# Kernel tuning notes

Hardware: AMD Instinct MI355X
Metric: run time of the kernel (lower is better)

## Reference

```python
import jax, jax.numpy as jnp
import numpy as np

# ---- static config (mirrors module init / config constants) ----
STATE_DIM = 512
D_H = 2048
INPUT_DIM = 1024
N_QUBITS = 6
N_VQC_LAYERS = 3
MSD = 128                 # mamba_state_dim (last dim of padded state)
PAD_SLICES = 16           # padded slice count in h_padded
MIN_T = 1e-6              # control_limits.min_value
REL_STEP = 0.1            # control_limits.hardware_relative_step
ABS_STEP = 1e-4           # control_limits.hardware_absolute_step
MAX_T = 0.05              # control_limits.max_value
DIM = 2 ** N_QUBITS

# qubit 0 = most significant bit (matches reshape-based gate application)
_BITS = ((np.arange(DIM)[:, None] >> np.arange(N_QUBITS)[None, ::-1]) & 1).astype(np.float32)
_sign = np.ones(DIM, np.float32)
for k in range(N_QUBITS):  # ring CZ entanglement
    k2 = (k + 1) % N_QUBITS
    _sign *= 1.0 - 2.0 * _BITS[:, k] * _BITS[:, k2]
CZ_SIGN = jnp.asarray(_sign)
Z_OBS = jnp.asarray((1.0 - 2.0 * _BITS).mean(axis=1))  # mean <Z_k> observable weights


def _apply_ry(state, ang, k):
    # state: [B, 2^n] real statevector; ang: [B] rotation angle on qubit k
    B = state.shape[0]
    s = state.reshape(B, 2 ** k, 2, 2 ** (N_QUBITS - k - 1))
    c = jnp.cos(ang / 2)[:, None, None]
    si = jnp.sin(ang / 2)[:, None, None]
    a0, a1 = s[:, :, 0, :], s[:, :, 1, :]
    out = jnp.stack([c * a0 - si * a1, si * a0 + c * a1], axis=2)
    return out.reshape(B, DIM)


def _vqc(feats, enc_W, enc_b, thetas):
    # EvolutionTimeVQCLayer: angle-encode features, layered RY + ring CZ, mean-Z expectation
    B = feats.shape[0]
    angles = feats @ enc_W + enc_b  # [B, n_qubits]
    state = jnp.zeros((B, DIM), feats.dtype).at[:, 0].set(1.0)
    for k in range(N_QUBITS):
        state = _apply_ry(state, angles[:, k], k)
    for l in range(N_VQC_LAYERS):
        for k in range(N_QUBITS):
            state = _apply_ry(state, jnp.broadcast_to(thetas[l, k], (B,)), k)
        state = state * CZ_SIGN[None, :]
    return (state * state) @ Z_OBS  # [B]


def _hamiltonian(q, p, x, W1, b1, W2, b2, W3, b3):
    z = jnp.concatenate([q, p, x], axis=-1)          # [B, 2*S + D]
    h1 = jnp.tanh(z @ W1 + b1)
    h2 = jnp.tanh(h1 @ W2 + b2)
    return (h2 @ W3)[:, 0] + b3                       # [B] scalar energy per sample


def setup_inputs() -> dict:
    key = jax.random.key(0)
    ks = jax.random.split(key, 12)
    def glorot(k, shape):
        std = np.sqrt(2.0 / (shape[0] + shape[-1]))
        return jax.random.normal(k, shape, jnp.float32) * std
    B = 2048
    h_in = 2 * STATE_DIM + INPUT_DIM
    gen_in = INPUT_DIM + 2 * STATE_DIM
    return {
        'x': jax.random.normal(ks[0], (B, INPUT_DIM), jnp.float32),
        'h_padded': jax.random.normal(ks[1], (B, PAD_SLICES, MSD), jnp.float32),
        'aux_padded': jnp.zeros((B, PAD_SLICES, MSD), jnp.float32),
        'W1': glorot(ks[2], (h_in, D_H)), 'b1': jnp.zeros((D_H,), jnp.float32),
        'W2': glorot(ks[3], (D_H, D_H)), 'b2': jnp.zeros((D_H,), jnp.float32),
        'W3': glorot(ks[4], (D_H, 1)), 'b3': jnp.zeros((), jnp.float32),
        'W_out': glorot(ks[5], (2 * STATE_DIM, INPUT_DIM)),
        'b_out': jnp.zeros((INPUT_DIM,), jnp.float32),
        'enc_W': glorot(ks[6], (gen_in, N_QUBITS)) * 0.1,
        'enc_b': jnp.zeros((N_QUBITS,), jnp.float32),
        'thetas': jax.random.normal(ks[7], (N_VQC_LAYERS, N_QUBITS), jnp.float32) * 0.1,
        'gain': jnp.asarray(0.1, jnp.float32),
        'shift': jnp.asarray(7.0, jnp.float32),
        'cap_param': jnp.asarray(0.02, jnp.float32),
        'time_bias': jnp.asarray(0.0005, jnp.float32),
        'last_stable': jnp.asarray(0.0005, jnp.float32),
    }


def reference(x, h_padded, aux_padded, W1, b1, W2, b2, W3, b3, W_out, b_out,
              enc_W, enc_b, thetas, gain, shift, cap_param, time_bias, last_stable):
    B = x.shape[0]
    total = 2 * STATE_DIM
    num_slices = total // MSD
    # unpack phase-space state from padded mamba-shaped state
    unpacked = h_padded[:, :num_slices, :].reshape(B, total)
    q_t, p_t = jnp.split(unpacked, 2, axis=-1)

    # ---- evolution-time generation via VQC ----
    ctrl = jnp.concatenate([x, q_t, p_t], axis=-1)
    samples = _vqc(ctrl, enc_W, enc_b, thetas)                       # [B]
    soft_gain = jax.nn.softplus(gain)
    soft_shift = jax.nn.softplus(shift)
    adjusted = jax.nn.softplus(soft_gain * samples - soft_shift)
    raw = jnp.mean(adjusted) + time_bias
    cap = jnp.maximum(jax.nn.softplus(cap_param), 1e-6)
    evo = cap * jax.nn.sigmoid(raw / cap)
    evo = jnp.where(jnp.isfinite(evo), evo, cap * jax.nn.sigmoid(time_bias / cap))
    prev = jnp.maximum(last_stable, MIN_T)
    cand = jnp.maximum(evo, MIN_T)
    max_step = jnp.maximum(prev * REL_STEP, ABS_STEP)
    cand = jnp.minimum(cand, prev + max_step)
    cand = jnp.minimum(cand, MAX_T)
    dt = jnp.where(jnp.isfinite(cand), cand, prev)                   # scalar

    # ---- fused HNN symplectic (leapfrog) step ----
    def H_sum(q, p):
        return _hamiltonian(q, p, x, W1, b1, W2, b2, W3, b3).sum()
    grad_qp = jax.grad(H_sum, argnums=(0, 1))
    dHdq0, _ = grad_qp(q_t, p_t)
    p_half = p_t - 0.5 * dt * dHdq0
    _, dHdp_h = grad_qp(q_t, p_half)
    q_next = q_t + dt * dHdp_h
    dHdq_n, _ = grad_qp(q_next, p_half)
    p_next = p_half - 0.5 * dt * dHdq_n

    out = jnp.concatenate([q_next, p_next], axis=-1) @ W_out + b_out  # [B, INPUT_DIM]

    # repack state into padded mamba layout
    new_slices = jnp.concatenate([q_next, p_next], axis=-1).reshape(B, num_slices, MSD)
    pad = jnp.zeros((B, PAD_SLICES - num_slices, MSD), out.dtype)
    h_next = jnp.concatenate([new_slices, pad], axis=1)
    return out, h_next
```

## Files before the change

kernel.cpp:

```cpp
#include <hip/hip_runtime.h>
#include <math.h>

#define NB 2048
#define ZD 2048
#define SD 512
#define NELEM_Z (NB * ZD)
#define MB_ (1024 * 1024)

typedef float f32x4 __attribute__((ext_vector_type(4)));
typedef __bf16 bf16x8 __attribute__((ext_vector_type(8)));
typedef __bf16 bf16x4 __attribute__((ext_vector_type(4)));
typedef long long i64;

__device__ __forceinline__ float softplus_f(float x) {
  if (x > 20.f) return x;
  if (x < -20.f) return expf(x);
  return log1pf(expf(x));
}

__device__ __forceinline__ void gload_lds16(const __bf16* g, __bf16* l) {
  __builtin_amdgcn_global_load_lds(
      (__attribute__((address_space(1))) void*)(g),
      (__attribute__((address_space(3))) void*)(l), 16, 0, 0);
}

__device__ __forceinline__ int pack_fp8x4(float a, float b, float c, float d) {
  int p = __builtin_amdgcn_cvt_pk_fp8_f32(a, b, 0, false);
  p = __builtin_amdgcn_cvt_pk_fp8_f32(c, d, p, true);
  return p;
}
__device__ __forceinline__ float fp8_to_f32(unsigned char b) {
  return __builtin_amdgcn_cvt_f32_fp8((int)b, 0);
}

__global__ __launch_bounds__(256) void build_z_kernel(
    const float* __restrict__ x,
    const float* __restrict__ h_padded,
    const float* __restrict__ enc_W,
    const float* __restrict__ enc_b,
    float* __restrict__ z,
    __bf16* __restrict__ zb,
    unsigned char* __restrict__ zf8,
    float* __restrict__ angles,
    float* __restrict__ acc) {
  int b = blockIdx.x;
  int tid = threadIdx.x;
  if (b == 0 && tid == 0) acc[0] = 0.f;
  int lane = tid & 63, w = tid >> 6;
  __shared__ float red[4][6];

  float pa[6] = {0.f, 0.f, 0.f, 0.f, 0.f, 0.f};
#pragma unroll
  for (int cc = 0; cc < 2; cc++) {
    int c = cc * 256 + tid;
    int i = c * 4;
    f32x4 v = (i < 1024) ? ((const f32x4*)(h_padded + (size_t)b * 2048))[c]
                         : ((const f32x4*)(x + (size_t)b * 1024))[c - 256];
    size_t zi = (size_t)b * 512 + c;
    ((f32x4*)z)[zi] = v;
    bf16x4 o;
    o[0] = (__bf16)v[0]; o[1] = (__bf16)v[1];
    o[2] = (__bf16)v[2]; o[3] = (__bf16)v[3];
    ((bf16x4*)zb)[zi] = o;
    ((int*)zf8)[zi] = pack_fp8x4(v[0], v[1], v[2], v[3]);
    int cj = (i < 1024) ? (1024 + i) : (i - 1024);
#pragma unroll
    for (int e = 0; e < 4; e++) {
      const float* wp = enc_W + (size_t)(cj + e) * 6;
#pragma unroll
      for (int k = 0; k < 6; k++) pa[k] += v[e] * wp[k];
    }
  }
#pragma unroll
  for (int k = 0; k < 6; k++)
    for (int off = 32; off > 0; off >>= 1) pa[k] += __shfl_down(pa[k], off, 64);
  if (lane == 0) {
#pragma unroll
    for (int k = 0; k < 6; k++) red[w][k] = pa[k];
  }
  __syncthreads();
  if (tid < 6)
    angles[b * 6 + tid] =
        red[0][tid] + red[1][tid] + red[2][tid] + red[3][tid] + enc_b[tid];
}

__global__ void prep_w(const float* __restrict__ in,
                       __bf16* __restrict__ outT, int R, int C) {
  __shared__ float tile[32][33];
  int bx = blockIdx.x * 32, by = blockIdx.y * 32;
  int tx = threadIdx.x, ty = threadIdx.y;
  for (int r = ty; r < 32; r += 8)
    tile[r][tx] = in[(size_t)(by + r) * C + bx + tx];
  __syncthreads();
  for (int r = ty; r < 32; r += 8)
    outT[(size_t)(bx + r) * R + by + tx] = (__bf16)tile[tx][r];
}

__global__ void prep_w8(const float* __restrict__ in,
                        unsigned char* __restrict__ outN,
                        unsigned char* __restrict__ outT, int R, int C) {
  __shared__ float tile[32][33];
  int bx = blockIdx.x * 32, by = blockIdx.y * 32;
  int tx = threadIdx.x, ty = threadIdx.y;
  for (int r = ty; r < 32; r += 8) {
    float v = in[(size_t)(by + r) * C + bx + tx] * 16.f;
    tile[r][tx] = v;
    int p = __builtin_amdgcn_cvt_pk_fp8_f32(v, v, 0, false);
    outN[(size_t)(by + r) * C + bx + tx] = (unsigned char)(p & 0xff);
  }
  __syncthreads();
  for (int r = ty; r < 32; r += 8) {
    float v = tile[tx][r];
    int p = __builtin_amdgcn_cvt_pk_fp8_f32(v, v, 0, false);
    outT[(size_t)(bx + r) * R + by + tx] = (unsigned char)(p & 0xff);
  }
}

__global__ __launch_bounds__(64) void sim_kernel(
    const float* __restrict__ angles,
    const float* __restrict__ thetas,
    const float* __restrict__ gain,
    const float* __restrict__ shift,
    float* __restrict__ acc) {
  int row = blockIdx.x * 64 + threadIdx.x;
  const float* a = angles + row * 6;

  float s[64];
#pragma unroll
  for (int i = 0; i < 64; i++) s[i] = 0.f;
  s[0] = 1.f;

#pragma unroll
  for (int k = 0; k < 6; k++) {
    float half = 0.5f * a[k];
    float c = cosf(half), si = sinf(half);
    int m = 1 << (5 - k);
#pragma unroll
    for (int i = 0; i < 64; i++) {
      if ((i & m) == 0) {
        float a0 = s[i], a1 = s[i | m];
        s[i] = c * a0 - si * a1;
        s[i | m] = si * a0 + c * a1;
      }
    }
  }
#pragma unroll
  for (int l = 0; l < 3; l++) {
#pragma unroll
    for (int k = 0; k < 6; k++) {
      float half = 0.5f * thetas[l * 6 + k];
      float c = cosf(half), si = sinf(half);
      int m = 1 << (5 - k);
#pragma unroll
      for (int i = 0; i < 64; i++) {
        if ((i & m) == 0) {
          float a0 = s[i], a1 = s[i | m];
          s[i] = c * a0 - si * a1;
          s[i | m] = si * a0 + c * a1;
        }
      }
    }
#pragma unroll
    for (int i = 0; i < 64; i++) {
      int rot = ((i << 1) | (i >> 5)) & 63;
      if (__popc(i & rot) & 1) s[i] = -s[i];
    }
  }

  float val = 0.f;
#pragma unroll
  for (int i = 0; i < 64; i++) {
    float zo = (6.f - 2.f * (float)__popc(i)) * (1.f / 6.f);
    val += s[i] * s[i] * zo;
  }
  float sg = softplus_f(gain[0]);
  float ss = softplus_f(shift[0]);
  float adj = softplus_f(sg * val - ss);
  for (int off = 32; off > 0; off >>= 1) adj += __shfl_down(adj, off, 64);
  if (threadIdx.x == 0) atomicAdd(acc, adj);
}

__global__ void dt_kernel(const float* __restrict__ acc,
                          const float* __restrict__ cap_param,
                          const float* __restrict__ time_bias,
                          const float* __restrict__ last_stable,
                          float* __restrict__ dt_out) {
  float raw = acc[0] * (1.f / (float)NB) + time_bias[0];
  float cap = fmaxf(softplus_f(cap_param[0]), 1e-6f);
  float evo = cap / (1.f + expf(-raw / cap));
  if (!isfinite(evo)) evo = cap / (1.f + expf(-time_bias[0] / cap));
  float prev = fmaxf(last_stable[0], 1e-6f);
  float cand = fmaxf(evo, 1e-6f);
  float max_step = fmaxf(prev * 0.1f, 1e-4f);
  cand = fminf(cand, prev + max_step);
  cand = fminf(cand, 0.05f);
  dt_out[0] = isfinite(cand) ? cand : prev;
}

template <int EPI>
__global__ __launch_bounds__(256, 2) void mfma_gemm8(
    const unsigned char* __restrict__ A, int lda,
    const unsigned char* __restrict__ Bt, int ldb,
    void* __restrict__ Cv, int ldc,
    const float* __restrict__ bias,
    const float* __restrict__ w3,
    const unsigned char* __restrict__ aux, int ldaux,
    int Kslice) {
  __shared__ __align__(16) unsigned char sA[2][128 * 144];
  __shared__ __align__(16) unsigned char sB[2][64 * 144];

  const int tid = threadIdx.x;
  const int lane = tid & 63;
  const int w = tid >> 6;
  const int wm = w & 1, wn = w >> 1;
  const int row0 = blockIdx.y * 128;
  const int col0 = blockIdx.x * 64;
  const int koff = blockIdx.z * Kslice;

  const unsigned char* gA[4]; int wA0[4], wA1[4];
  const unsigned char* gB[2]; int wB0[2], wB1[2];
#pragma unroll
  for (int i = 0; i < 4; i++) {
    int c = i * 256 + tid;
    int m = c >> 3, cp = c & 7;
    gA[i] = A + (size_t)(row0 + m) * lda + koff + cp * 16;
    int h = cp >> 1;
    int Hofs = (h >> 1) * 16 + (h & 1) * 8;
    wA0[i] = m * 144 + ((2 * cp) & 3) * 32 + Hofs;
    wA1[i] = m * 144 + ((2 * cp + 1) & 3) * 32 + Hofs;
  }
#pragma unroll
  for (int i = 0; i < 2; i++) {
    int c = i * 256 + tid;
    int m = c >> 3, cp = c & 7;
    gB[i] = Bt + (size_t)(col0 + m) * ldb + koff + cp * 16;
    int h = cp >> 1;
    int Hofs = (h >> 1) * 16 + (h & 1) * 8;
    wB0[i] = m * 144 + ((2 * cp) & 3) * 32 + Hofs;
    wB1[i] = m * 144 + ((2 * cp + 1) & 3) * 32 + Hofs;
  }

  const int q = lane >> 4, r = lane & 15;
  int aoff[4][2], boff[2][2];
#pragma unroll
  for (int i = 0; i < 4; i++) {
    int ma = wm * 64 + i * 16 + r;
#pragma unroll
    for (int H = 0; H < 2; H++) aoff[i][H] = ma * 144 + q * 32 + H * 16;
  }
#pragma unroll
  for (int j = 0; j < 2; j++) {
    int mb = wn * 32 + j * 16 + r;
#pragma unroll
    for (int H = 0; H < 2; H++) boff[j][H] = mb * 144 + q * 32 + H * 16;
  }

  f32x4 acc[4][2] = {};
  f32x4 rA[4], rB[2];

#pragma unroll
  for (int i = 0; i < 4; i++) rA[i] = *(const f32x4*)gA[i];
#pragma unroll
  for (int i = 0; i < 2; i++) rB[i] = *(const f32x4*)gB[i];
#pragma unroll
  for (int i = 0; i < 4; i++) {
    *(i64*)(&sA[0][0] + wA0[i]) = ((const i64*)&rA[i])[0];
    *(i64*)(&sA[0][0] + wA1[i]) = ((const i64*)&rA[i])[1];
  }
#pragma unroll
  for (int i = 0; i < 2; i++) {
    *(i64*)(&sB[0][0] + wB0[i]) = ((const i64*)&rB[i])[0];
    *(i64*)(&sB[0][0] + wB1[i]) = ((const i64*)&rB[i])[1];
  }
  __syncthreads();

  int cur = 0;
  for (int k0 = 0; k0 < Kslice; k0 += 128) {
    const bool more = (k0 + 128 < Kslice);
    if (more) {
#pragma unroll
      for (int i = 0; i < 4; i++) rA[i] = *(const f32x4*)(gA[i] + k0 + 128);
#pragma unroll
      for (int i = 0; i < 2; i++) rB[i] = *(const f32x4*)(gB[i] + k0 + 128);
    }

    const unsigned char* bA = &sA[cur][0];
    const unsigned char* bB = &sB[cur][0];
#pragma unroll
    for (int H = 0; H < 2; H++) {
      i64 a0[4], a1[4], b0[2], b1[2];
#pragma unroll
      for (int i = 0; i < 4; i++) {
        f32x4 v = *(const f32x4*)(bA + aoff[i][H]);
        a0[i] = ((const i64*)&v)[0];
        a1[i] = ((const i64*)&v)[1];
      }
#pragma unroll
      for (int j = 0; j < 2; j++) {
        f32x4 v = *(const f32x4*)(bB + boff[j][H]);
        b0[j] = ((const i64*)&v)[0];
        b1[j] = ((const i64*)&v)[1];
      }
#pragma unroll
      for (int i = 0; i < 4; i++)
#pragma unroll
        for (int j = 0; j < 2; j++)
          acc[i][j] = __builtin_amdgcn_mfma_f32_16x16x32_fp8_fp8(
              a0[i], b0[j], acc[i][j], 0, 0, 0);
#pragma unroll
      for (int i = 0; i < 4; i++)
#pragma unroll
        for (int j = 0; j < 2; j++)
          acc[i][j] = __builtin_amdgcn_mfma_f32_16x16x32_fp8_fp8(
              a1[i], b1[j], acc[i][j], 0, 0, 0);
    }

    if (more) {
      unsigned char* nA = &sA[cur ^ 1][0];
      unsigned char* nB = &sB[cur ^ 1][0];
#pragma unroll
      for (int i = 0; i < 4; i++) {
        *(i64*)(nA + wA0[i]) = ((const i64*)&rA[i])[0];
        *(i64*)(nA + wA1[i]) = ((const i64*)&rA[i])[1];
      }
#pragma unroll
      for (int i = 0; i < 2; i++) {
        *(i64*)(nB + wB0[i]) = ((const i64*)&rB[i])[0];
        *(i64*)(nB + wB1[i]) = ((const i64*)&rB[i])[1];
      }
    }
    __syncthreads();
    cur ^= 1;
  }

  float* Cf = (float*)Cv;
  unsigned char* C8 = (unsigned char*)Cv;
  float* Pz = Cf + (size_t)blockIdx.z * (size_t)gridDim.y * 128 * ldc;

#pragma unroll
  for (int i = 0; i < 4; i++) {
    int rowb = row0 + wm * 64 + i * 16 + q * 4;
#pragma unroll
    for (int j = 0; j < 2; j++) {
      int col = col0 + wn * 32 + j * 16 + r;
      if (EPI == 0) {
#pragma unroll
        for (int g = 0; g < 4; g++)
          Pz[(size_t)(rowb + g) * ldc + col] = acc[i][j][g];
      } else {
        float o[4];
#pragma unroll
        for (int g = 0; g < 4; g++) {
          float v = acc[i][j][g] * 0.0625f;
          if (EPI == 1) {
            o[g] = tanhf(v + bias[col]);
          } else if (EPI == 2) {
            float t = tanhf(v + bias[col]);
            o[g] = 32.f * (1.f - t * t) * w3[col];
          } else {
            float h = fp8_to_f32(aux[(size_t)(rowb + g) * ldaux + col]);
            o[g] = v * (1.f - h * h);
          }
        }
        int p = pack_fp8x4(o[0], o[1], o[2], o[3]);
#pragma unroll
        for (int g = 0; g < 4; g++)
          C8[(size_t)(rowb + g) * ldc + col] =
              (unsigned char)((p >> (8 * g)) & 0xff);
      }
    }
  }
}

__global__ __launch_bounds__(256, 2) void mfma_gemm_bf16(
    const __bf16* __restrict__ A, int lda,
    const __bf16* __restrict__ Bt, int ldb,
    float* __restrict__ P, int ldc,
    int Kslice) {
  __shared__ __bf16 sA[2][128 * 64];
  __shared__ __bf16 sB[2][64 * 64];

  const int tid = threadIdx.x;
  const int lane = tid & 63;
  const int w = tid >> 6;
  const int wm = w & 1, wn = w >> 1;
  const int row0 = blockIdx.y * 128;
  const int col0 = blockIdx.x * 64;
  const int koff = blockIdx.z * Kslice;

  const __bf16* gA[4]; int lofA[4];
  const __bf16* gB[2]; int lofB[2];
#pragma unroll
  for (int i = 0; i < 4; i++) {
    int c = i * 256 + tid;
    int m = c >> 3, cc = c & 7;
    int o = cc ^ (m & 7);
    gA[i] = A + (size_t)(row0 + m) * lda + koff + o * 8;
    lofA[i] = c * 8;
  }
#pragma unroll
  for (int i = 0; i < 2; i++) {
    int c = i * 256 + tid;
    int m = c >> 3, cc = c & 7;
    int o = cc ^ (m & 7);
    gB[i] = Bt + (size_t)(col0 + m) * ldb + koff + o * 8;
    lofB[i] = c * 8;
  }

  const int q = lane >> 4, r = lane & 15;
  int aoff[4][2], boff[2][2];
#pragma unroll
  for (int i = 0; i < 4; i++) {
    int ma = wm * 64 + i * 16 + r;
#pragma unroll
    for (int h = 0; h < 2; h++)
      aoff[i][h] = (ma * 8 + ((h * 4 + q) ^ (ma & 7))) * 8;
  }
#pragma unroll
  for (int j = 0; j < 2; j++) {
    int mb = wn * 32 + j * 16 + r;
#pragma unroll
    for (int h = 0; h < 2; h++)
      boff[j][h] = (mb * 8 + ((h * 4 + q) ^ (mb & 7))) * 8;
  }

  f32x4 acc[4][2] = {};

#pragma unroll
  for (int i = 0; i < 4; i++) gload_lds16(gA[i], &sA[0][0] + lofA[i]);
#pragma unroll
  for (int i = 0; i < 2; i++) gload_lds16(gB[i], &sB[0][0] + lofB[i]);

  int cur = 0;
  for (int k0 = 0; k0 < Kslice; k0 += 64) {
    __syncthreads();
    if (k0 + 64 < Kslice) {
      int nxt = cur ^ 1;
#pragma unroll
      for (int i = 0; i < 4; i++)
        gload_lds16(gA[i] + k0 + 64, &sA[nxt][0] + lofA[i]);
#pragma unroll
      for (int i = 0; i < 2; i++)
        gload_lds16(gB[i] + k0 + 64, &sB[nxt][0] + lofB[i]);
    }
#pragma unroll
    for (int h = 0; h < 2; h++) {
      bf16x8 af[4], bfr[2];
#pragma unroll
      for (int i = 0; i < 4; i++)
        af[i] = *(const bf16x8*)(&sA[cur][0] + aoff[i][h]);
#pragma unroll
      for (int j = 0; j < 2; j++)
        bfr[j] = *(const bf16x8*)(&sB[cur][0] + boff[j][h]);
#pragma unroll
      for (int i = 0; i < 4; i++)
#pragma unroll
        for (int j = 0; j < 2; j++)
          acc[i][j] = __builtin_amdgcn_mfma_f32_16x16x32_bf16(af[i], bfr[j],
                                                              acc[i][j], 0, 0, 0);
    }
    cur ^= 1;
  }

  float* Pz = P + (size_t)blockIdx.z * (size_t)gridDim.y * 128 * ldc;
#pragma unroll
  for (int i = 0; i < 4; i++) {
    int rowb = row0 + wm * 64 + i * 16 + q * 4;
#pragma unroll
    for (int j = 0; j < 2; j++) {
      int col = col0 + wn * 32 + j * 16 + r;
#pragma unroll
      for (int g = 0; g < 4; g++)
        Pz[(size_t)(rowb + g) * ldc + col] = acc[i][j][g];
    }
  }
}

__global__ void update_kernel(float* __restrict__ z, __bf16* __restrict__ zb,
                              unsigned char* __restrict__ zf8,
                              const float* __restrict__ gp,
                              const float* __restrict__ dt,
                              float coef, int off) {
  int t = blockIdx.x * blockDim.x + threadIdx.x;
  int b = t >> 7;
  int j4 = t & 127;
  const f32x4* g4 = (const f32x4*)gp;
  constexpr int STRIDE = NB * SD / 4;
  f32x4 g = g4[t] + g4[t + STRIDE] + g4[t + 2 * STRIDE] + g4[t + 3 * STRIDE];
  int zi4 = (b * ZD + off) / 4 + j4;
  f32x4 v = ((f32x4*)z)[zi4];
  float s = coef * dt[0] * (1.f / 512.f);
  v[0] += s * g[0]; v[1] += s * g[1]; v[2] += s * g[2]; v[3] += s * g[3];
  ((f32x4*)z)[zi4] = v;
  bf16x4 o;
  o[0] = (__bf16)v[0]; o[1] = (__bf16)v[1];
  o[2] = (__bf16)v[2]; o[3] = (__bf16)v[3];
  ((bf16x4*)zb)[zi4] = o;
  ((int*)zf8)[zi4] = pack_fp8x4(v[0], v[1], v[2], v[3]);
}

__global__ void wout_reduce(const float* __restrict__ gp,
                            const float* __restrict__ b_out,
                            float* __restrict__ out) {
  int t = blockIdx.x * blockDim.x + threadIdx.x;
  constexpr int S = NB * 1024 / 4;
  const f32x4* g4 = (const f32x4*)gp;
  f32x4 v = g4[t] + g4[t + S];
  f32x4 bb = ((const f32x4*)b_out)[t & 255];
  v[0] += bb[0]; v[1] += bb[1]; v[2] += bb[2]; v[3] += bb[3];
  ((f32x4*)out)[t] = v;
}

__global__ void hnext_kernel(const float* __restrict__ z,
                             float* __restrict__ out) {
  int t = blockIdx.x * blockDim.x + threadIdx.x;
  int i4 = t & 511;
  f32x4 zero = {0.f, 0.f, 0.f, 0.f};
  ((f32x4*)out)[t] = (i4 < 256) ? ((const f32x4*)z)[t] : zero;
}

extern "C" void kernel_launch(void* const* d_in, const int* in_sizes, int n_in,
                              void* d_out, int out_size, void* d_ws,
                              size_t ws_size, hipStream_t stream) {
  const float* x        = (const float*)d_in[0];
  const float* h_padded = (const float*)d_in[1];
  const float* W1    = (const float*)d_in[3];
  const float* b1    = (const float*)d_in[4];
  const float* W2    = (const float*)d_in[5];
  const float* b2    = (const float*)d_in[6];
  const float* W3    = (const float*)d_in[7];
  const float* W_out = (const float*)d_in[9];
  const float* b_out = (const float*)d_in[10];
  const float* enc_W = (const float*)d_in[11];
  const float* enc_b = (const float*)d_in[12];
  const float* thetas = (const float*)d_in[13];
  const float* gain   = (const float*)d_in[14];
  const float* shift  = (const float*)d_in[15];
  const float* cap_p  = (const float*)d_in[16];
  const float* t_bias = (const float*)d_in[17];
  const float* l_stab = (const float*)d_in[18];

  float* out_mat  = (float*)d_out;
  float* out_hnxt = (float*)d_out + NB * 1024;

  char* base = (char*)d_ws;
  float* z      = (float*)(base);
  float* part   = (float*)(base + 16 * MB_);
  __bf16* zb    = (__bf16*)(base + 32 * MB_);
  __bf16* Wot   = (__bf16*)(base + 40 * MB_);
  float* angl   = (float*)(base + 42 * MB_);
  float* accp   = (float*)(base + 42 * MB_ + 65536);
  float* dtp    = accp + 1;
  unsigned char* zf8  = (unsigned char*)(base + 43 * MB_);
  unsigned char* h1_8 = zf8 + (size_t)NELEM_Z;
  unsigned char* g2_8 = h1_8 + (size_t)NELEM_Z;
  unsigned char* g1_8 = g2_8 + (size_t)NELEM_Z;
  unsigned char* W1n8 = g1_8 + (size_t)NELEM_Z;
  unsigned char* W1t8 = W1n8 + (size_t)NELEM_Z;
  unsigned char* W2n8 = W1t8 + (size_t)NELEM_Z;
  unsigned char* W2t8 = W2n8 + (size_t)NELEM_Z;

  dim3 thr256(256);
  dim3 thrT(32, 8);

  prep_w8<<<dim3(64, 64), thrT, 0, stream>>>(W1, W1n8, W1t8, ZD, ZD);
  prep_w8<<<dim3(64, 64), thrT, 0, stream>>>(W2, W2n8, W2t8, ZD, ZD);
  prep_w<<<dim3(32, 32), thrT, 0, stream>>>(W_out, Wot, 1024, 1024);

  build_z_kernel<<<dim3(NB), thr256, 0, stream>>>(x, h_padded, enc_W, enc_b, z,
                                                  zb, zf8, angl, accp);
  sim_kernel<<<dim3(NB / 64), dim3(64), 0, stream>>>(angl, thetas, gain, shift,
                                                     accp);
  dt_kernel<<<dim3(1), dim3(1), 0, stream>>>(accp, cap_p, t_bias, l_stab, dtp);

  const int   j0r[3]  = {0, 512, 0};
  const int   offs[3] = {512, 0, 512};
  const float coef[3] = {-0.5f, 1.0f, -0.5f};

  dim3 gridSq(32, 16, 1);
  dim3 gridGr(8, 16, 4);

  for (int i = 0; i < 3; i++) {
    mfma_gemm8<1><<<gridSq, thr256, 0, stream>>>(
        zf8, ZD, W1t8, ZD, h1_8, ZD, b1, nullptr, nullptr, 0, ZD);
    mfma_gemm8<2><<<gridSq, thr256, 0, stream>>>(
        h1_8, ZD, W2t8, ZD, g2_8, ZD, b2, W3, nullptr, 0, ZD);
    mfma_gemm8<3><<<gridSq, thr256, 0, stream>>>(
        g2_8, ZD, W2n8, ZD, g1_8, ZD, nullptr, nullptr, h1_8, ZD, ZD);
    mfma_gemm8<0><<<gridGr, thr256, 0, stream>>>(
        g1_8, ZD, W1n8 + (size_t)j0r[i] * ZD, ZD, part, SD, nullptr, nullptr,
        nullptr, 0, 512);
    update_kernel<<<dim3(NB * SD / 4 / 256), thr256, 0, stream>>>(
        z, zb, zf8, part, dtp, coef[i], offs[i]);
  }

  mfma_gemm_bf16<<<dim3(16, 16, 2), thr256, 0, stream>>>(zb, ZD, Wot, 1024,
                                                         part, 1024, 512);
  wout_reduce<<<dim3(NB * 1024 / 4 / 256), thr256, 0, stream>>>(part, b_out,
                                                                out_mat);

  hnext_kernel<<<dim3(NELEM_Z / 4 / 256), thr256, 0, stream>>>(z, out_hnxt);
}
```

Measured before the change: 447.1 us.

## Use MX-scaled 16x16x128 FP8 MFMA with XOR-swizzled unpadded LDS tiles

Replaces the pairs of 16x16x32 FP8 MFMAs with the gfx950 scaled 16x16x128 f8f6f4 MFMA, using neutral scale exponents, so each k-tile needs one matrix instruction per output fragment. The LDS layout moves from 144-byte padded rows with split 8-byte stores to 128-byte rows with an XOR swizzle, which allows single 16-byte stores and reads. This is meant to cut MFMA issue count and LDS instruction overhead. It depends on the operand lane/K mapping of the new instruction matching the swizzled layout, or the results will be wrong.

```diff
diff --git a/kernel.cpp b/kernel.cpp
--- a/kernel.cpp
+++ b/kernel.cpp
@@ -10,6 +10,8 @@
 typedef float f32x4 __attribute__((ext_vector_type(4)));
 typedef __bf16 bf16x8 __attribute__((ext_vector_type(8)));
 typedef __bf16 bf16x4 __attribute__((ext_vector_type(4)));
+typedef int i32x4 __attribute__((ext_vector_type(4)));
+typedef int i32x8 __attribute__((ext_vector_type(8)));
 typedef long long i64;
 
 __device__ __forceinline__ float softplus_f(float x) {
@@ -206,8 +208,8 @@
     const float* __restrict__ w3,
     const unsigned char* __restrict__ aux, int ldaux,
     int Kslice) {
-  __shared__ __align__(16) unsigned char sA[2][128 * 144];
-  __shared__ __align__(16) unsigned char sB[2][64 * 144];
+  __shared__ __align__(16) unsigned char sA[2][128 * 128];
+  __shared__ __align__(16) unsigned char sB[2][64 * 128];
 
   const int tid = threadIdx.x;
   const int lane = tid & 63;
@@ -217,27 +219,21 @@
   const int col0 = blockIdx.x * 64;
   const int koff = blockIdx.z * Kslice;
 
-  const unsigned char* gA[4]; int wA0[4], wA1[4];
-  const unsigned char* gB[2]; int wB0[2], wB1[2];
+  const unsigned char* gA[4]; int wA[4];
+  const unsigned char* gB[2]; int wB[2];
 #pragma unroll
   for (int i = 0; i < 4; i++) {
     int c = i * 256 + tid;
-    int m = c >> 3, cp = c & 7;
-    gA[i] = A + (size_t)(row0 + m) * lda + koff + cp * 16;
-    int h = cp >> 1;
-    int Hofs = (h >> 1) * 16 + (h & 1) * 8;
-    wA0[i] = m * 144 + ((2 * cp) & 3) * 32 + Hofs;
-    wA1[i] = m * 144 + ((2 * cp + 1) & 3) * 32 + Hofs;
+    int m = c >> 3, s = c & 7;
+    gA[i] = A + (size_t)(row0 + m) * lda + koff + s * 16;
+    wA[i] = m * 128 + ((s ^ (m & 7)) << 4);
   }
 #pragma unroll
   for (int i = 0; i < 2; i++) {
     int c = i * 256 + tid;
-    int m = c >> 3, cp = c & 7;
-    gB[i] = Bt + (size_t)(col0 + m) * ldb + koff + cp * 16;
-    int h = cp >> 1;
-    int Hofs = (h >> 1) * 16 + (h & 1) * 8;
-    wB0[i] = m * 144 + ((2 * cp) & 3) * 32 + Hofs;
-    wB1[i] = m * 144 + ((2 * cp + 1) & 3) * 32 + Hofs;
+    int m = c >> 3, s = c & 7;
+    gB[i] = Bt + (size_t)(col0 + m) * ldb + koff + s * 16;
+    wB[i] = m * 128 + ((s ^ (m & 7)) << 4);
   }
 
   const int q = lane >> 4, r = lane & 15;
@@ -246,13 +242,15 @@
   for (int i = 0; i < 4; i++) {
     int ma = wm * 64 + i * 16 + r;
 #pragma unroll
-    for (int H = 0; H < 2; H++) aoff[i][H] = ma * 144 + q * 32 + H * 16;
+    for (int H = 0; H < 2; H++)
+      aoff[i][H] = ma * 128 + (((2 * q + H) ^ (ma & 7)) << 4);
   }
 #pragma unroll
   for (int j = 0; j < 2; j++) {
     int mb = wn * 32 + j * 16 + r;
 #pragma unroll
-    for (int H = 0; H < 2; H++) boff[j][H] = mb * 144 + q * 32 + H * 16;
+    for (int H = 0; H < 2; H++)
+      boff[j][H] = mb * 128 + (((2 * q + H) ^ (mb & 7)) << 4);
   }
 
   f32x4 acc[4][2] = {};
@@ -263,15 +261,9 @@
 #pragma unroll
   for (int i = 0; i < 2; i++) rB[i] = *(const f32x4*)gB[i];
 #pragma unroll
-  for (int i = 0; i < 4; i++) {
-    *(i64*)(&sA[0][0] + wA0[i]) = ((const i64*)&rA[i])[0];
-    *(i64*)(&sA[0][0] + wA1[i]) = ((const i64*)&rA[i])[1];
-  }
-#pragma unroll
-  for (int i = 0; i < 2; i++) {
-    *(i64*)(&sB[0][0] + wB0[i]) = ((const i64*)&rB[i])[0];
-    *(i64*)(&sB[0][0] + wB1[i]) = ((const i64*)&rB[i])[1];
-  }
+  for (int i = 0; i < 4; i++) *(f32x4*)(&sA[0][0] + wA[i]) = rA[i];
+#pragma unroll
+  for (int i = 0; i < 2; i++) *(f32x4*)(&sB[0][0] + wB[i]) = rB[i];
   __syncthreads();
 
   int cur = 0;
@@ -286,48 +278,34 @@
 
     const unsigned char* bA = &sA[cur][0];
     const unsigned char* bB = &sB[cur][0];
-#pragma unroll
-    for (int H = 0; H < 2; H++) {
-      i64 a0[4], a1[4], b0[2], b1[2];
-#pragma unroll
-      for (int i = 0; i < 4; i++) {
-        f32x4 v = *(const f32x4*)(bA + aoff[i][H]);
-        a0[i] = ((const i64*)&v)[0];
-        a1[i] = ((const i64*)&v)[1];
-      }
-#pragma unroll
-      for (int j = 0; j < 2; j++) {
-        f32x4 v = *(const f32x4*)(bB + boff[j][H]);
-        b0[j] = ((const i64*)&v)[0];
-        b1[j] = ((const i64*)&v)[1];
-      }
-#pragma unroll
-      for (int i = 0; i < 4; i++)
-#pragma unroll
-        for (int j = 0; j < 2; j++)
-          acc[i][j] = __builtin_amdgcn_mfma_f32_16x16x32_fp8_fp8(
-              a0[i], b0[j], acc[i][j], 0, 0, 0);
-#pragma unroll
-      for (int i = 0; i < 4; i++)
-#pragma unroll
-        for (int j = 0; j < 2; j++)
-          acc[i][j] = __builtin_amdgcn_mfma_f32_16x16x32_fp8_fp8(
-              a1[i], b1[j], acc[i][j], 0, 0, 0);
-    }
+    i32x8 af[4], bfr[2];
+#pragma unroll
+    for (int i = 0; i < 4; i++) {
+      i32x4 lo = *(const i32x4*)(bA + aoff[i][0]);
+      i32x4 hi = *(const i32x4*)(bA + aoff[i][1]);
+      af[i] = __builtin_shufflevector(lo, hi, 0, 1, 2, 3, 4, 5, 6, 7);
+    }
+#pragma unroll
+    for (int j = 0; j < 2; j++) {
+      i32x4 lo = *(const i32x4*)(bB + boff[j][0]);
+      i32x4 hi = *(const i32x4*)(bB + boff[j][1]);
+      bfr[j] = __builtin_shufflevector(lo, hi, 0, 1, 2, 3, 4, 5, 6, 7);
+    }
+#pragma unroll
+    for (int i = 0; i < 4; i++)
+#pragma unroll
+      for (int j = 0; j < 2; j++)
+        acc[i][j] = __builtin_amdgcn_mfma_scale_f32_16x16x128_f8f6f4(
+            af[i], bfr[j], acc[i][j], 0 , 0 ,
+            0, 0x7F7F7F7F, 0, 0x7F7F7F7F);
 
     if (more) {
       unsigned char* nA = &sA[cur ^ 1][0];
       unsigned char* nB = &sB[cur ^ 1][0];
 #pragma unroll
-      for (int i = 0; i < 4; i++) {
-        *(i64*)(nA + wA0[i]) = ((const i64*)&rA[i])[0];
-        *(i64*)(nA + wA1[i]) = ((const i64*)&rA[i])[1];
-      }
-#pragma unroll
-      for (int i = 0; i < 2; i++) {
-        *(i64*)(nB + wB0[i]) = ((const i64*)&rB[i])[0];
-        *(i64*)(nB + wB1[i]) = ((const i64*)&rB[i])[1];
-      }
+      for (int i = 0; i < 4; i++) *(f32x4*)(nA + wA[i]) = rA[i];
+#pragma unroll
+      for (int i = 0; i < 2; i++) *(f32x4*)(nB + wB[i]) = rB[i];
     }
     __syncthreads();
     cur ^= 1;
```

Result: slower. 474.2 us (+6.1%).
